# Kernel tuning notes

Measured on AMD Instinct MI355X. Metric: run time of the kernel, lower is better.

Reference implementation:

```python
import jax, jax.numpy as jnp
import numpy as np

M = 131072  # KV length
DK = 256    # key dim
DV = 256    # value dim


def setup_inputs() -> dict:
    key = jax.random.key(0)
    k1, k2, k3 = jax.random.split(key, 3)
    q = jax.random.normal(k1, (DK,), dtype=jnp.float32)
    K = jax.random.normal(k2, (M, DK), dtype=jnp.float32)
    V = jax.random.normal(k3, (M, DV), dtype=jnp.float32)
    return {"q": q, "K": K, "V": V}


def reference(q, K, V):
    # logits[m] = sum_k K[m,k] * q[k]
    logits = jnp.einsum('mk,k->m', K, q)
    # stable softmax over the m axis
    weights = jax.nn.softmax(logits, axis=-1)
    # y[v] = sum_m weights[m] * V[m,v]
    return jnp.einsum('m,mv->v', weights, V)
```

## Files before the change

### kernel.cpp

```cpp
#include <hip/hip_runtime.h>
#include <math.h>

#define DKD 256
#define DVD 256

constexpr int TPB   = 256;
constexpr int NB    = 1024;
constexpr int RPB   = 128;
constexpr int RED_B = 64;

typedef float floatx4 __attribute__((ext_vector_type(4)));

__device__ __forceinline__ float4 ntload4(const float4* p) {
    floatx4 v = __builtin_nontemporal_load((const floatx4*)p);
    return make_float4(v.x, v.y, v.z, v.w);
}

__global__ __launch_bounds__(TPB, 4) void k_logits(
    const float* __restrict__ q,
    const float* __restrict__ K,
    float* __restrict__ logits,
    int M)
{
    const int lane = threadIdx.x & 63;
    const int wave = threadIdx.x >> 6;
    const float4* __restrict__ K4 = (const float4*)K;
    const float4 q4 = ((const float4*)q)[lane];

    const int wbeg = blockIdx.x * RPB + wave * (RPB / 4);

    #pragma unroll 2
    for (int it = 0; it < (RPB / 4) / 4; ++it) {
        const int r = wbeg + it * 4;
        if (r >= M) break;
        const size_t base = (size_t)r * 64 + lane;
        float4 k0 = ntload4(&K4[base]);
        float4 k1 = ntload4(&K4[base + 64]);
        float4 k2 = ntload4(&K4[base + 128]);
        float4 k3 = ntload4(&K4[base + 192]);

        float s0 = k0.x*q4.x + k0.y*q4.y + k0.z*q4.z + k0.w*q4.w;
        float s1 = k1.x*q4.x + k1.y*q4.y + k1.z*q4.z + k1.w*q4.w;
        float s2 = k2.x*q4.x + k2.y*q4.y + k2.z*q4.z + k2.w*q4.w;
        float s3 = k3.x*q4.x + k3.y*q4.y + k3.z*q4.z + k3.w*q4.w;

        #pragma unroll
        for (int off = 32; off > 0; off >>= 1) {
            s0 += __shfl_xor(s0, off);
            s1 += __shfl_xor(s1, off);
            s2 += __shfl_xor(s2, off);
            s3 += __shfl_xor(s3, off);
        }
        if (lane < 4) {
            const float sv = lane == 0 ? s0 : lane == 1 ? s1 : lane == 2 ? s2 : s3;
            if (r + lane < M) logits[r + lane] = sv;
        }
    }
}

__global__ __launch_bounds__(TPB) void k_max(
    const float* __restrict__ logits, float* __restrict__ pmax, int M)
{
    __shared__ float red[TPB];
    const int t = threadIdx.x;
    const float4* L4 = (const float4*)logits;
    const int n4 = M / 4;
    float lm = -INFINITY;
    for (int i = blockIdx.x * TPB + t; i < n4; i += RED_B * TPB) {
        const float4 v = L4[i];
        lm = fmaxf(lm, fmaxf(fmaxf(v.x, v.y), fmaxf(v.z, v.w)));
    }
    red[t] = lm; __syncthreads();
    for (int s = TPB / 2; s > 0; s >>= 1) {
        if (t < s) red[t] = fmaxf(red[t], red[t + s]);
        __syncthreads();
    }
    if (t == 0) pmax[blockIdx.x] = red[0];
}

__global__ __launch_bounds__(TPB) void k_expsum(
    const float* __restrict__ logits,
    const float* __restrict__ pmax,
    float* __restrict__ w,
    float* __restrict__ psum,
    int M)
{
    __shared__ float red[TPB];
    const int t = threadIdx.x;

    float lm = (t < RED_B) ? pmax[t] : -INFINITY;
    red[t] = lm; __syncthreads();
    for (int s = TPB / 2; s > 0; s >>= 1) {
        if (t < s) red[t] = fmaxf(red[t], red[t + s]);
        __syncthreads();
    }
    const float Mg = red[0];
    __syncthreads();

    const float4* L4 = (const float4*)logits;
    float4* W4 = (float4*)w;
    const int n4 = M / 4;
    float ls = 0.f;
    for (int i = blockIdx.x * TPB + t; i < n4; i += RED_B * TPB) {
        const float4 v = L4[i];
        float4 e;
        e.x = __expf(v.x - Mg); e.y = __expf(v.y - Mg);
        e.z = __expf(v.z - Mg); e.w = __expf(v.w - Mg);
        W4[i] = e;
        ls += e.x + e.y + e.z + e.w;
    }
    red[t] = ls; __syncthreads();
    for (int s = TPB / 2; s > 0; s >>= 1) {
        if (t < s) red[t] += red[t + s];
        __syncthreads();
    }
    if (t == 0) psum[blockIdx.x] = red[0];
}

__global__ __launch_bounds__(TPB, 4) void k_vacc(
    const float* __restrict__ V,
    const float* __restrict__ w,
    float* __restrict__ partT,
    int M)
{
    __shared__ float4 s_acc[4][64];
    const int t    = threadIdx.x;
    const int lane = t & 63;
    const int wave = t >> 6;
    const int b    = blockIdx.x;
    const float4* __restrict__ V4 = (const float4*)V;
    const float4* __restrict__ W4 = (const float4*)w;

    const int wbeg = b * RPB + wave * (RPB / 4);
    float4 acc = make_float4(0.f, 0.f, 0.f, 0.f);

    #pragma unroll 2
    for (int it = 0; it < (RPB / 4) / 4; ++it) {
        const int r = wbeg + it * 4;
        if (r >= M) break;
        const size_t base = (size_t)r * 64 + lane;
        const float4 w4 = W4[r >> 2];
        float4 v0 = ntload4(&V4[base]);
        float4 v1 = ntload4(&V4[base + 64]);
        float4 v2 = ntload4(&V4[base + 128]);
        float4 v3 = ntload4(&V4[base + 192]);

        acc.x += w4.x*v0.x + w4.y*v1.x + w4.z*v2.x + w4.w*v3.x;
        acc.y += w4.x*v0.y + w4.y*v1.y + w4.z*v2.y + w4.w*v3.y;
        acc.z += w4.x*v0.z + w4.y*v1.z + w4.z*v2.z + w4.w*v3.z;
        acc.w += w4.x*v0.w + w4.y*v1.w + w4.z*v2.w + w4.w*v3.w;
    }

    s_acc[wave][lane] = acc;
    __syncthreads();
    float yv = 0.f;
    const float* saf = (const float*)&s_acc[0][0];
    #pragma unroll
    for (int ww = 0; ww < 4; ++ww) yv += saf[ww * DVD + t];
    partT[(size_t)t * NB + b] = yv;
}

__global__ __launch_bounds__(TPB) void k_combine(
    const float* __restrict__ partT,
    const float* __restrict__ psum,
    float* __restrict__ out)
{
    __shared__ float red[TPB];
    const int t = threadIdx.x;

    float ls = (t < RED_B) ? psum[t] : 0.f;
    red[t] = ls; __syncthreads();
    for (int s = TPB / 2; s > 0; s >>= 1) {
        if (t < s) red[t] += red[t + s];
        __syncthreads();
    }
    const float invL = 1.0f / red[0];
    __syncthreads();

    const int j = blockIdx.x;
    const float4* P4 = (const float4*)(partT + (size_t)j * NB);
    float part = 0.f;
    const float4 v = P4[t];
    part = v.x + v.y + v.z + v.w;
    red[t] = part; __syncthreads();
    for (int s = TPB / 2; s > 0; s >>= 1) {
        if (t < s) red[t] += red[t + s];
        __syncthreads();
    }
    if (t == 0) out[j] = red[0] * invL;
}

extern "C" void kernel_launch(void* const* d_in, const int* in_sizes, int n_in,
                              void* d_out, int out_size, void* d_ws, size_t ws_size,
                              hipStream_t stream) {
    const float* q = (const float*)d_in[0];
    const float* K = (const float*)d_in[1];
    const float* V = (const float*)d_in[2];
    float* out = (float*)d_out;

    const int M = in_sizes[1] / DKD;

    float* ws     = (float*)d_ws;
    float* logits = ws;
    float* w      = logits + M;
    float* partT  = w + M;
    float* pmax   = partT + (size_t)DVD * NB;
    float* psum   = pmax + RED_B;

    k_logits <<<NB,    TPB, 0, stream>>>(q, K, logits, M);
    k_max    <<<RED_B, TPB, 0, stream>>>(logits, pmax, M);
    k_expsum <<<RED_B, TPB, 0, stream>>>(logits, pmax, w, psum, M);
    k_vacc   <<<NB,    TPB, 0, stream>>>(V, w, partT, M);
    k_combine<<<DVD,   TPB, 0, stream>>>(partT, psum, out);
}
```

Measured before the change: 266.2 us.

## Fuse logits, softmax and V accumulation into one split-softmax kernel

Replaces the five-kernel pipeline with a single fused kernel. Each block computes its 128 logits into shared memory, takes a local max and exp-sum, and accumulates V weighted by the local exponentials. A combine kernel then rescales the per-block partials by exp(local max minus global max), as in flash-decoding. This removes the logits and weights round-trips through global memory and three kernel launches, but drops the nontemporal load hints and the M bounds checks, so it assumes M equals NB*RPB.

```diff
diff --git a/kernel.cpp b/kernel.cpp
--- a/kernel.cpp
+++ b/kernel.cpp
@@ -4,40 +4,42 @@
 #define DKD 256
 #define DVD 256
 
-constexpr int TPB   = 256;
-constexpr int NB    = 1024;
-constexpr int RPB   = 128;
-constexpr int RED_B = 64;
+constexpr int TPB = 256;
+constexpr int NB  = 1024;
+constexpr int RPB = 128;
 
-typedef float floatx4 __attribute__((ext_vector_type(4)));
-
-__device__ __forceinline__ float4 ntload4(const float4* p) {
-    floatx4 v = __builtin_nontemporal_load((const floatx4*)p);
-    return make_float4(v.x, v.y, v.z, v.w);
-}
-
-__global__ __launch_bounds__(TPB, 4) void k_logits(
+__global__ __launch_bounds__(TPB, 4) void k_fused(
     const float* __restrict__ q,
     const float* __restrict__ K,
-    float* __restrict__ logits,
-    int M)
+    const float* __restrict__ V,
+    float* __restrict__ partT,
+    float* __restrict__ pmax,
+    float* __restrict__ psum)
 {
-    const int lane = threadIdx.x & 63;
-    const int wave = threadIdx.x >> 6;
+    __shared__ __align__(16) float s_l[RPB];
+    __shared__ float  s_wred[4];
+    __shared__ float4 s_acc[4][64];
+
+    const int t    = threadIdx.x;
+    const int lane = t & 63;
+    const int wave = t >> 6;
+    const int b    = blockIdx.x;
+
     const float4* __restrict__ K4 = (const float4*)K;
+    const float4* __restrict__ V4 = (const float4*)V;
     const float4 q4 = ((const float4*)q)[lane];
 
-    const int wbeg = blockIdx.x * RPB + wave * (RPB / 4);
+    const int wbeg = b * RPB + wave * (RPB / 4);
 
+    float wmax = -INFINITY;
     #pragma unroll 2
-    for (int it = 0; it < (RPB / 4) / 4; ++it) {
+    for (int it = 0; it < 8; ++it) {
         const int r = wbeg + it * 4;
-        if (r >= M) break;
         const size_t base = (size_t)r * 64 + lane;
-        float4 k0 = ntload4(&K4[base]);
-        float4 k1 = ntload4(&K4[base + 64]);
-        float4 k2 = ntload4(&K4[base + 128]);
-        float4 k3 = ntload4(&K4[base + 192]);
+        float4 k0 = K4[base];
+        float4 k1 = K4[base + 64];
+        float4 k2 = K4[base + 128];
+        float4 k3 = K4[base + 192];
 
         float s0 = k0.x*q4.x + k0.y*q4.y + k0.z*q4.z + k0.w*q4.w;
         float s1 = k1.x*q4.x + k1.y*q4.y + k1.z*q4.z + k1.w*q4.w;
@@ -51,99 +53,37 @@
             s2 += __shfl_xor(s2, off);
             s3 += __shfl_xor(s3, off);
         }
+        wmax = fmaxf(wmax, fmaxf(fmaxf(s0, s1), fmaxf(s2, s3)));
         if (lane < 4) {
             const float sv = lane == 0 ? s0 : lane == 1 ? s1 : lane == 2 ? s2 : s3;
-            if (r + lane < M) logits[r + lane] = sv;
+            s_l[wave * 32 + it * 4 + lane] = sv;
         }
     }
-}
-
-__global__ __launch_bounds__(TPB) void k_max(
-    const float* __restrict__ logits, float* __restrict__ pmax, int M)
-{
-    __shared__ float red[TPB];
-    const int t = threadIdx.x;
-    const float4* L4 = (const float4*)logits;
-    const int n4 = M / 4;
-    float lm = -INFINITY;
-    for (int i = blockIdx.x * TPB + t; i < n4; i += RED_B * TPB) {
-        const float4 v = L4[i];
-        lm = fmaxf(lm, fmaxf(fmaxf(v.x, v.y), fmaxf(v.z, v.w)));
-    }
-    red[t] = lm; __syncthreads();
-    for (int s = TPB / 2; s > 0; s >>= 1) {
-        if (t < s) red[t] = fmaxf(red[t], red[t + s]);
-        __syncthreads();
-    }
-    if (t == 0) pmax[blockIdx.x] = red[0];
-}
-
-__global__ __launch_bounds__(TPB) void k_expsum(
-    const float* __restrict__ logits,
-    const float* __restrict__ pmax,
-    float* __restrict__ w,
-    float* __restrict__ psum,
-    int M)
-{
-    __shared__ float red[TPB];
-    const int t = threadIdx.x;
-
-    float lm = (t < RED_B) ? pmax[t] : -INFINITY;
-    red[t] = lm; __syncthreads();
-    for (int s = TPB / 2; s > 0; s >>= 1) {
-        if (t < s) red[t] = fmaxf(red[t], red[t + s]);
-        __syncthreads();
-    }
-    const float Mg = red[0];
+    if (lane == 0) s_wred[wave] = wmax;
     __syncthreads();
 
-    const float4* L4 = (const float4*)logits;
-    float4* W4 = (float4*)w;
-    const int n4 = M / 4;
-    float ls = 0.f;
-    for (int i = blockIdx.x * TPB + t; i < n4; i += RED_B * TPB) {
-        const float4 v = L4[i];
-        float4 e;
-        e.x = __expf(v.x - Mg); e.y = __expf(v.y - Mg);
-        e.z = __expf(v.z - Mg); e.w = __expf(v.w - Mg);
-        W4[i] = e;
-        ls += e.x + e.y + e.z + e.w;
+    const float mb = fmaxf(fmaxf(s_wred[0], s_wred[1]), fmaxf(s_wred[2], s_wred[3]));
+
+    if (t < RPB) s_l[t] = __expf(s_l[t] - mb);
+    __syncthreads();
+    if (wave == 0) {
+        float es = s_l[lane] + s_l[lane + 64];
+        #pragma unroll
+        for (int off = 32; off > 0; off >>= 1) es += __shfl_xor(es, off);
+        if (lane == 0) { pmax[b] = mb; psum[b] = es; }
     }
-    red[t] = ls; __syncthreads();
-    for (int s = TPB / 2; s > 0; s >>= 1) {
-        if (t < s) red[t] += red[t + s];
-        __syncthreads();
-    }
-    if (t == 0) psum[blockIdx.x] = red[0];
-}
 
-__global__ __launch_bounds__(TPB, 4) void k_vacc(
-    const float* __restrict__ V,
-    const float* __restrict__ w,
-    float* __restrict__ partT,
-    int M)
-{
-    __shared__ float4 s_acc[4][64];
-    const int t    = threadIdx.x;
-    const int lane = t & 63;
-    const int wave = t >> 6;
-    const int b    = blockIdx.x;
-    const float4* __restrict__ V4 = (const float4*)V;
-    const float4* __restrict__ W4 = (const float4*)w;
-
-    const int wbeg = b * RPB + wave * (RPB / 4);
     float4 acc = make_float4(0.f, 0.f, 0.f, 0.f);
-
+    const int ebase = wave * 32;
     #pragma unroll 2
-    for (int it = 0; it < (RPB / 4) / 4; ++it) {
+    for (int it = 0; it < 8; ++it) {
         const int r = wbeg + it * 4;
-        if (r >= M) break;
         const size_t base = (size_t)r * 64 + lane;
-        const float4 w4 = W4[r >> 2];
-        float4 v0 = ntload4(&V4[base]);
-        float4 v1 = ntload4(&V4[base + 64]);
-        float4 v2 = ntload4(&V4[base + 128]);
-        float4 v3 = ntload4(&V4[base + 192]);
+        const float4 w4 = *(const float4*)&s_l[ebase + it * 4];
+        float4 v0 = V4[base];
+        float4 v1 = V4[base + 64];
+        float4 v2 = V4[base + 128];
+        float4 v3 = V4[base + 192];
 
         acc.x += w4.x*v0.x + w4.y*v1.x + w4.z*v2.x + w4.w*v3.x;
         acc.y += w4.x*v0.y + w4.y*v1.y + w4.z*v2.y + w4.w*v3.y;
@@ -162,14 +102,31 @@
 
 __global__ __launch_bounds__(TPB) void k_combine(
     const float* __restrict__ partT,
+    const float* __restrict__ pmax,
     const float* __restrict__ psum,
     float* __restrict__ out)
 {
     __shared__ float red[TPB];
+    __shared__ __align__(16) float s_a[NB];
     const int t = threadIdx.x;
 
-    float ls = (t < RED_B) ? psum[t] : 0.f;
-    red[t] = ls; __syncthreads();
+    const float4 pm = ((const float4*)pmax)[t];
+    float lm = fmaxf(fmaxf(pm.x, pm.y), fmaxf(pm.z, pm.w));
+    red[t] = lm; __syncthreads();
+    for (int s = TPB / 2; s > 0; s >>= 1) {
+        if (t < s) red[t] = fmaxf(red[t], red[t + s]);
+        __syncthreads();
+    }
+    const float Mg = red[0];
+    __syncthreads();
+
+    const float4 ps = ((const float4*)psum)[t];
+    float4 a;
+    a.x = __expf(pm.x - Mg); a.y = __expf(pm.y - Mg);
+    a.z = __expf(pm.z - Mg); a.w = __expf(pm.w - Mg);
+    ((float4*)s_a)[t] = a;
+    red[t] = a.x*ps.x + a.y*ps.y + a.z*ps.z + a.w*ps.w;
+    __syncthreads();
     for (int s = TPB / 2; s > 0; s >>= 1) {
         if (t < s) red[t] += red[t + s];
         __syncthreads();
@@ -178,11 +135,10 @@
     __syncthreads();
 
     const int j = blockIdx.x;
-    const float4* P4 = (const float4*)(partT + (size_t)j * NB);
-    float part = 0.f;
-    const float4 v = P4[t];
-    part = v.x + v.y + v.z + v.w;
-    red[t] = part; __syncthreads();
+    const float4 v  = ((const float4*)(partT + (size_t)j * NB))[t];
+    const float4 av = ((const float4*)s_a)[t];
+    red[t] = v.x*av.x + v.y*av.y + v.z*av.z + v.w*av.w;
+    __syncthreads();
     for (int s = TPB / 2; s > 0; s >>= 1) {
         if (t < s) red[t] += red[t + s];
         __syncthreads();
@@ -198,18 +154,11 @@
     const float* V = (const float*)d_in[2];
     float* out = (float*)d_out;
 
-    const int M = in_sizes[1] / DKD;
+    float* ws    = (float*)d_ws;
+    float* partT = ws;
+    float* pmax  = partT + (size_t)DVD * NB;
+    float* psum  = pmax + NB;
 
-    float* ws     = (float*)d_ws;
-    float* logits = ws;
-    float* w      = logits + M;
-    float* partT  = w + M;
-    float* pmax   = partT + (size_t)DVD * NB;
-    float* psum   = pmax + RED_B;
-
-    k_logits <<<NB,    TPB, 0, stream>>>(q, K, logits, M);
-    k_max    <<<RED_B, TPB, 0, stream>>>(logits, pmax, M);
-    k_expsum <<<RED_B, TPB, 0, stream>>>(logits, pmax, w, psum, M);
-    k_vacc   <<<NB,    TPB, 0, stream>>>(V, w, partT, M);
-    k_combine<<<DVD,   TPB, 0, stream>>>(partT, psum, out);
+    k_fused  <<<NB,  TPB, 0, stream>>>(q, K, V, partT, pmax, psum);
+    k_combine<<<DVD, TPB, 0, stream>>>(partT, pmax, psum, out);
 }
```

Measured after the change: 280.5 us. 1.05x slower.
